# Optimization experiments

Measured on AMD Instinct MI355X. Metric: run time of the kernel, lower is better.

The kernel has to match this reference:

```python
import jax, jax.numpy as jnp
import numpy as np
from jax import lax

D_MODEL = 1024
D_STATE = 16
BATCH = 4
SEQ = 2048
EPS = 1e-5


def setup_inputs() -> dict:
    key = jax.random.key(0)
    ks = jax.random.split(key, 5)
    x = jax.random.normal(ks[0], (BATCH, SEQ, D_MODEL), dtype=jnp.float32)
    A_log = jax.random.normal(ks[1], (D_MODEL, D_STATE), dtype=jnp.float32) * 0.1
    # nn.Linear default init ~ U(-1/sqrt(fan_in), 1/sqrt(fan_in))
    B_w = jax.random.uniform(ks[2], (D_STATE, D_MODEL), minval=-1.0, maxval=1.0) / np.sqrt(D_MODEL)
    C_w = jax.random.uniform(ks[3], (D_MODEL, D_STATE), minval=-1.0, maxval=1.0) / np.sqrt(D_STATE)
    D = jnp.ones((D_MODEL,), dtype=jnp.float32)
    gamma = jnp.ones((D_MODEL,), dtype=jnp.float32)
    beta = jnp.zeros((D_MODEL,), dtype=jnp.float32)
    return {"x": x, "A_log": A_log, "B_w": B_w, "C_w": C_w, "D": D, "gamma": gamma, "beta": beta}


def _layernorm(y, gamma, beta):
    mu = jnp.mean(y, axis=-1, keepdims=True)
    var = jnp.mean((y - mu) ** 2, axis=-1, keepdims=True)
    return (y - mu) * lax.rsqrt(var + EPS) * gamma + beta


def reference(x, A_log, B_w, C_w, D, gamma, beta):
    batch, seq_len, d = x.shape
    decay = jnp.exp(-jnp.exp(A_log))  # (d_model, d_state), exp(A) with A = -exp(A_log)
    # Precompute all B projections: (batch, seq, d_state)
    bx = jnp.einsum('bsd,nd->bsn', x, B_w)
    bx_t = jnp.swapaxes(bx, 0, 1)  # (seq, batch, d_state)

    def step(h, b_t):
        # h: (batch, d_model, d_state); b_t broadcast over d_model dim
        h = h * decay + b_t[:, None, :]
        return h, h.mean(axis=1)  # carry, per-step mean (batch, d_state)

    h0 = jnp.zeros((batch, d, A_log.shape[1]), dtype=x.dtype)
    _, hmeans = lax.scan(step, h0, bx_t)  # hmeans: (seq, batch, d_state)

    y = jnp.einsum('sbn,dn->bsd', hmeans, C_w) + D * x  # (batch, seq, d_model)
    return _layernorm(y, gamma, beta)
```

## Files before the change

kernel.cpp:

```cpp
#include <hip/hip_runtime.h>
#include <hip/hip_bf16.h>

#define D_MODEL 1024
#define D_STATE 16
#define BATCH   4
#define SEQ     2048
#define ROWS    (BATCH*SEQ)
#define WIN     64

#define K1_ROWS 8
__global__ __launch_bounds__(256, 4) void k_bx(const float* __restrict__ x,
                                               const float* __restrict__ Bw,
                                               float* __restrict__ bx) {
    __shared__ float xs[K1_ROWS][1024];
    __shared__ float red[4][8][K1_ROWS][2];
    const int tid  = threadIdx.x;
    const int np   = tid & 7;
    const int dblk = tid >> 3;
    const int row0 = blockIdx.x * K1_ROWS;
    const int lane = tid & 63, wid = tid >> 6;

    float4 bw0[8], bw1[8];
    {
        const float4* p0 = reinterpret_cast<const float4*>(Bw + (size_t)(2 * np    ) * 1024 + dblk * 32);
        const float4* p1 = reinterpret_cast<const float4*>(Bw + (size_t)(2 * np + 1) * 1024 + dblk * 32);
#pragma unroll
        for (int j = 0; j < 8; ++j) { bw0[j] = p0[j]; bw1[j] = p1[j]; }
    }

    const int chunk = tid >> 3;
    const int slotw = ((tid & 7) + chunk) & 7;
#pragma unroll
    for (int r = 0; r < K1_ROWS; ++r) {
        float4 v = reinterpret_cast<const float4*>(x + (size_t)(row0 + r) * 1024)[tid];
        *reinterpret_cast<float4*>(&xs[r][chunk * 32 + slotw * 4]) = v;
    }
    __syncthreads();

    float a0[K1_ROWS], a1[K1_ROWS];
#pragma unroll
    for (int r = 0; r < K1_ROWS; ++r) { a0[r] = 0.f; a1[r] = 0.f; }

#pragma unroll
    for (int r = 0; r < K1_ROWS; ++r) {
#pragma unroll
        for (int j = 0; j < 8; ++j) {
            const int slot = (j + dblk) & 7;
            float4 xv = *reinterpret_cast<const float4*>(&xs[r][dblk * 32 + slot * 4]);
            a0[r] = fmaf(xv.x, bw0[j].x, a0[r]); a0[r] = fmaf(xv.y, bw0[j].y, a0[r]);
            a0[r] = fmaf(xv.z, bw0[j].z, a0[r]); a0[r] = fmaf(xv.w, bw0[j].w, a0[r]);
            a1[r] = fmaf(xv.x, bw1[j].x, a1[r]); a1[r] = fmaf(xv.y, bw1[j].y, a1[r]);
            a1[r] = fmaf(xv.z, bw1[j].z, a1[r]); a1[r] = fmaf(xv.w, bw1[j].w, a1[r]);
        }
    }

#pragma unroll
    for (int r = 0; r < K1_ROWS; ++r) {
        float v0 = a0[r], v1 = a1[r];
        v0 += __shfl_xor(v0, 8);  v1 += __shfl_xor(v1, 8);
        v0 += __shfl_xor(v0, 16); v1 += __shfl_xor(v1, 16);
        v0 += __shfl_xor(v0, 32); v1 += __shfl_xor(v1, 32);
        a0[r] = v0; a1[r] = v1;
    }
    if (lane < 8) {
#pragma unroll
        for (int r = 0; r < K1_ROWS; ++r) {
            red[wid][lane][r][0] = a0[r];
            red[wid][lane][r][1] = a1[r];
        }
    }
    __syncthreads();
    if (tid < K1_ROWS * 16) {
        const int r = tid >> 4, n = tid & 15;
        float v = red[0][n >> 1][r][n & 1] + red[1][n >> 1][r][n & 1]
                + red[2][n >> 1][r][n & 1] + red[3][n >> 1][r][n & 1];
        bx[(size_t)(row0 + r) * D_STATE + n] = v;
    }
}

__global__ __launch_bounds__(256) void k_kbar(const float* __restrict__ A_log,
                                              float* __restrict__ KbarT) {
    const int n = blockIdx.x;
    const int tid = threadIdx.x;
    const int delta = tid & 63;
    const int c     = tid >> 6;
    __shared__ float l2[D_MODEL];
    __shared__ float red[4][WIN];

    for (int d = tid; d < D_MODEL; d += 256) {
        float a = A_log[d * D_STATE + n];
        l2[d] = -expf(a) * 1.4426950408889634f;
    }
    __syncthreads();

    const float fdelta = (float)delta;
    float acc = 0.f;
    const int d0 = c * 256;
    for (int d = d0; d < d0 + 256; ++d)
        acc += exp2f(fdelta * l2[d]);
    red[c][delta] = acc;
    __syncthreads();
    if (tid < WIN)
        KbarT[tid * D_STATE + n] =
            (red[0][tid] + red[1][tid] + red[2][tid] + red[3][tid]) * (1.0f / 1024.0f);
}

__global__ __launch_bounds__(256) void k_fir(const float* __restrict__ bx,
                                             const float* __restrict__ KbarT,
                                             float* __restrict__ hm) {
    __shared__ float4 kb4[WIN][4];
    const int tid = threadIdx.x;
    kb4[tid >> 2][tid & 3] = reinterpret_cast<const float4*>(KbarT)[tid];
    __syncthreads();

    const int nq  = tid & 3;
    const int row = blockIdx.x * 64 + (tid >> 2);
    const int t   = row & (SEQ - 1);
    const float4* bp = reinterpret_cast<const float4*>(bx + (size_t)row * D_STATE) + nq;
    float4 acc = {0.f, 0.f, 0.f, 0.f};
    if (t >= WIN - 1) {
#pragma unroll
        for (int dl = 0; dl < WIN; ++dl) {
            float4 b = bp[-(ptrdiff_t)dl * 4];
            float4 k = kb4[dl][nq];
            acc.x = fmaf(k.x, b.x, acc.x); acc.y = fmaf(k.y, b.y, acc.y);
            acc.z = fmaf(k.z, b.z, acc.z); acc.w = fmaf(k.w, b.w, acc.w);
        }
    } else {
        for (int dl = 0; dl <= t; ++dl) {
            float4 b = bp[-(ptrdiff_t)dl * 4];
            float4 k = kb4[dl][nq];
            acc.x = fmaf(k.x, b.x, acc.x); acc.y = fmaf(k.y, b.y, acc.y);
            acc.z = fmaf(k.z, b.z, acc.z); acc.w = fmaf(k.w, b.w, acc.w);
        }
    }
    reinterpret_cast<float4*>(hm + (size_t)row * D_STATE)[nq] = acc;
}

#define KO_ROWS 4
__global__ __launch_bounds__(256, 4) void k_out(const float* __restrict__ x,
                                                const float* __restrict__ hm,
                                                const float* __restrict__ Cw,
                                                const float* __restrict__ Dp,
                                                const float* __restrict__ gamma,
                                                const float* __restrict__ beta,
                                                float* __restrict__ out) {
    const int tid = threadIdx.x;
    const int row0 = blockIdx.x * KO_ROWS;
    const int lane = tid & 63, wid = tid >> 6;
    __shared__ float red_s[KO_ROWS][4], red_q[KO_ROWS][4];

    float4 cw[4][4];
#pragma unroll
    for (int j = 0; j < 4; ++j) {
        const float4* p = reinterpret_cast<const float4*>(Cw + (size_t)(tid * 4 + j) * D_STATE);
#pragma unroll
        for (int q = 0; q < 4; ++q) cw[j][q] = p[q];
    }
    const float4 Dq = reinterpret_cast<const float4*>(Dp)[tid];
    const float4 gq = reinterpret_cast<const float4*>(gamma)[tid];
    const float4 bq = reinterpret_cast<const float4*>(beta)[tid];

    float4 y[KO_ROWS];
#pragma unroll
    for (int r = 0; r < KO_ROWS; ++r) {
        const size_t row = row0 + r;
        const float4* hp = reinterpret_cast<const float4*>(hm + row * D_STATE);
        const float4 h0 = hp[0], h1 = hp[1], h2 = hp[2], h3 = hp[3];
        const float4 xq = reinterpret_cast<const float4*>(x + row * D_MODEL)[tid];

        float4 v;
#pragma unroll
        for (int j = 0; j < 4; ++j) {
            float a = 0.f;
            a = fmaf(h0.x, cw[j][0].x, a); a = fmaf(h0.y, cw[j][0].y, a);
            a = fmaf(h0.z, cw[j][0].z, a); a = fmaf(h0.w, cw[j][0].w, a);
            a = fmaf(h1.x, cw[j][1].x, a); a = fmaf(h1.y, cw[j][1].y, a);
            a = fmaf(h1.z, cw[j][1].z, a); a = fmaf(h1.w, cw[j][1].w, a);
            a = fmaf(h2.x, cw[j][2].x, a); a = fmaf(h2.y, cw[j][2].y, a);
            a = fmaf(h2.z, cw[j][2].z, a); a = fmaf(h2.w, cw[j][2].w, a);
            a = fmaf(h3.x, cw[j][3].x, a); a = fmaf(h3.y, cw[j][3].y, a);
            a = fmaf(h3.z, cw[j][3].z, a); a = fmaf(h3.w, cw[j][3].w, a);
            ((float*)&v)[j] = a;
        }
        v.x = fmaf(Dq.x, xq.x, v.x);
        v.y = fmaf(Dq.y, xq.y, v.y);
        v.z = fmaf(Dq.z, xq.z, v.z);
        v.w = fmaf(Dq.w, xq.w, v.w);
        y[r] = v;

        float s  = v.x + v.y + v.z + v.w;
        float sq = v.x*v.x + v.y*v.y + v.z*v.z + v.w*v.w;
        s += __shfl_xor(s, 1);  sq += __shfl_xor(sq, 1);
        s += __shfl_xor(s, 2);  sq += __shfl_xor(sq, 2);
        s += __shfl_xor(s, 4);  sq += __shfl_xor(sq, 4);
        s += __shfl_xor(s, 8);  sq += __shfl_xor(sq, 8);
        s += __shfl_xor(s, 16); sq += __shfl_xor(sq, 16);
        s += __shfl_xor(s, 32); sq += __shfl_xor(sq, 32);
        if (lane == 0) { red_s[r][wid] = s; red_q[r][wid] = sq; }
    }
    __syncthreads();

#pragma unroll
    for (int r = 0; r < KO_ROWS; ++r) {
        const size_t row = row0 + r;
        const float ssum = red_s[r][0] + red_s[r][1] + red_s[r][2] + red_s[r][3];
        const float ssq  = red_q[r][0] + red_q[r][1] + red_q[r][2] + red_q[r][3];
        const float mu   = ssum * (1.0f / 1024.0f);
        const float var  = ssq * (1.0f / 1024.0f) - mu * mu;
        const float inv  = rsqrtf(var + 1e-5f);
        const float4 v = y[r];
        float4 o;
        o.x = fmaf((v.x - mu) * inv, gq.x, bq.x);
        o.y = fmaf((v.y - mu) * inv, gq.y, bq.y);
        o.z = fmaf((v.z - mu) * inv, gq.z, bq.z);
        o.w = fmaf((v.w - mu) * inv, gq.w, bq.w);
        reinterpret_cast<float4*>(out + row * D_MODEL)[tid] = o;
    }
}

extern "C" void kernel_launch(void* const* d_in, const int* in_sizes, int n_in,
                              void* d_out, int out_size, void* d_ws, size_t ws_size,
                              hipStream_t stream) {
    (void)in_sizes; (void)n_in; (void)out_size; (void)ws_size;
    const float* x     = (const float*)d_in[0];
    const float* A_log = (const float*)d_in[1];
    const float* B_w   = (const float*)d_in[2];
    const float* C_w   = (const float*)d_in[3];
    const float* Dp    = (const float*)d_in[4];
    const float* gamma = (const float*)d_in[5];
    const float* beta  = (const float*)d_in[6];
    float* out = (float*)d_out;

    float* bx = (float*)d_ws;
    float* kb = bx + (size_t)ROWS * D_STATE;
    float* hm = kb + WIN * D_STATE;

    k_bx  <<<ROWS / K1_ROWS, 256, 0, stream>>>(x, B_w, bx);
    k_kbar<<<D_STATE,        256, 0, stream>>>(A_log, kb);
    k_fir <<<ROWS / 64,      256, 0, stream>>>(bx, kb, hm);
    k_out <<<ROWS / KO_ROWS, 256, 0, stream>>>(x, hm, C_w, Dp, gamma, beta, out);
}
```

Before: 57.76 us.

## Fuse kernel-bar into projection kernel and FIR into output layernorm kernel

Merges the four-kernel pipeline into two launches. The decay-kernel computation now runs as extra blocks of the projection kernel, reusing its shared memory. The FIR convolution over the 64-step window is folded into the output/layernorm kernel, with each block computing its rows' state means into shared memory. This removes two launches and the hm round-trip through global memory, at the cost of redundant kbar loads per block. It also drops the occupancy hint on the projection kernel.

```diff
diff --git a/kernel.cpp b/kernel.cpp
--- a/kernel.cpp
+++ b/kernel.cpp
@@ -9,12 +9,40 @@
 #define WIN     64
 
 #define K1_ROWS 8
-__global__ __launch_bounds__(256, 4) void k_bx(const float* __restrict__ x,
-                                               const float* __restrict__ Bw,
-                                               float* __restrict__ bx) {
+__global__ __launch_bounds__(256) void k_proj(const float* __restrict__ x,
+                                              const float* __restrict__ Bw,
+                                              const float* __restrict__ A_log,
+                                              float* __restrict__ bx,
+                                              float* __restrict__ KbarT) {
     __shared__ float xs[K1_ROWS][1024];
     __shared__ float red[4][8][K1_ROWS][2];
-    const int tid  = threadIdx.x;
+    const int tid = threadIdx.x;
+
+    if (blockIdx.x >= ROWS / K1_ROWS) {
+        const int n = blockIdx.x - ROWS / K1_ROWS;
+        float* l2   = &xs[0][0];
+        float* kred = &xs[1][0];
+        const int delta = tid & 63;
+        const int c     = tid >> 6;
+        for (int d = tid; d < D_MODEL; d += 256) {
+            float a = A_log[d * D_STATE + n];
+            l2[d] = -expf(a) * 1.4426950408889634f;
+        }
+        __syncthreads();
+        const float fdelta = (float)delta;
+        float acc = 0.f;
+        const int d0 = c * 256;
+        for (int d = d0; d < d0 + 256; ++d)
+            acc += exp2f(fdelta * l2[d]);
+        kred[c * WIN + delta] = acc;
+        __syncthreads();
+        if (tid < WIN)
+            KbarT[tid * D_STATE + n] =
+                (kred[tid] + kred[WIN + tid] + kred[2 * WIN + tid] + kred[3 * WIN + tid])
+                * (1.0f / 1024.0f);
+        return;
+    }
+
     const int np   = tid & 7;
     const int dblk = tid >> 3;
     const int row0 = blockIdx.x * K1_ROWS;
@@ -78,77 +106,23 @@
     }
 }
 
-__global__ __launch_bounds__(256) void k_kbar(const float* __restrict__ A_log,
-                                              float* __restrict__ KbarT) {
-    const int n = blockIdx.x;
+#define KB_ROWS 4
+__global__ __launch_bounds__(256, 4) void k_fused(const float* __restrict__ x,
+                                                  const float* __restrict__ bxg,
+                                                  const float* __restrict__ KbarT,
+                                                  const float* __restrict__ Cw,
+                                                  const float* __restrict__ Dp,
+                                                  const float* __restrict__ gamma,
+                                                  const float* __restrict__ beta,
+                                                  float* __restrict__ out) {
     const int tid = threadIdx.x;
-    const int delta = tid & 63;
-    const int c     = tid >> 6;
-    __shared__ float l2[D_MODEL];
-    __shared__ float red[4][WIN];
-
-    for (int d = tid; d < D_MODEL; d += 256) {
-        float a = A_log[d * D_STATE + n];
-        l2[d] = -expf(a) * 1.4426950408889634f;
-    }
-    __syncthreads();
-
-    const float fdelta = (float)delta;
-    float acc = 0.f;
-    const int d0 = c * 256;
-    for (int d = d0; d < d0 + 256; ++d)
-        acc += exp2f(fdelta * l2[d]);
-    red[c][delta] = acc;
-    __syncthreads();
-    if (tid < WIN)
-        KbarT[tid * D_STATE + n] =
-            (red[0][tid] + red[1][tid] + red[2][tid] + red[3][tid]) * (1.0f / 1024.0f);
-}
-
-__global__ __launch_bounds__(256) void k_fir(const float* __restrict__ bx,
-                                             const float* __restrict__ KbarT,
-                                             float* __restrict__ hm) {
-    __shared__ float4 kb4[WIN][4];
-    const int tid = threadIdx.x;
-    kb4[tid >> 2][tid & 3] = reinterpret_cast<const float4*>(KbarT)[tid];
-    __syncthreads();
-
-    const int nq  = tid & 3;
-    const int row = blockIdx.x * 64 + (tid >> 2);
-    const int t   = row & (SEQ - 1);
-    const float4* bp = reinterpret_cast<const float4*>(bx + (size_t)row * D_STATE) + nq;
-    float4 acc = {0.f, 0.f, 0.f, 0.f};
-    if (t >= WIN - 1) {
-#pragma unroll
-        for (int dl = 0; dl < WIN; ++dl) {
-            float4 b = bp[-(ptrdiff_t)dl * 4];
-            float4 k = kb4[dl][nq];
-            acc.x = fmaf(k.x, b.x, acc.x); acc.y = fmaf(k.y, b.y, acc.y);
-            acc.z = fmaf(k.z, b.z, acc.z); acc.w = fmaf(k.w, b.w, acc.w);
-        }
-    } else {
-        for (int dl = 0; dl <= t; ++dl) {
-            float4 b = bp[-(ptrdiff_t)dl * 4];
-            float4 k = kb4[dl][nq];
-            acc.x = fmaf(k.x, b.x, acc.x); acc.y = fmaf(k.y, b.y, acc.y);
-            acc.z = fmaf(k.z, b.z, acc.z); acc.w = fmaf(k.w, b.w, acc.w);
-        }
-    }
-    reinterpret_cast<float4*>(hm + (size_t)row * D_STATE)[nq] = acc;
-}
-
-#define KO_ROWS 4
-__global__ __launch_bounds__(256, 4) void k_out(const float* __restrict__ x,
-                                                const float* __restrict__ hm,
-                                                const float* __restrict__ Cw,
-                                                const float* __restrict__ Dp,
-                                                const float* __restrict__ gamma,
-                                                const float* __restrict__ beta,
-                                                float* __restrict__ out) {
-    const int tid = threadIdx.x;
-    const int row0 = blockIdx.x * KO_ROWS;
+    const int row0 = blockIdx.x * KB_ROWS;
     const int lane = tid & 63, wid = tid >> 6;
-    __shared__ float red_s[KO_ROWS][4], red_q[KO_ROWS][4];
+    __shared__ float kb[WIN * D_STATE];
+    __shared__ float hm_s[KB_ROWS][D_STATE];
+    __shared__ float red_s[KB_ROWS][4], red_q[KB_ROWS][4];
+
+    reinterpret_cast<float4*>(kb)[tid] = reinterpret_cast<const float4*>(KbarT)[tid];
 
     float4 cw[4][4];
 #pragma unroll
@@ -160,12 +134,40 @@
     const float4 Dq = reinterpret_cast<const float4*>(Dp)[tid];
     const float4 gq = reinterpret_cast<const float4*>(gamma)[tid];
     const float4 bq = reinterpret_cast<const float4*>(beta)[tid];
-
-    float4 y[KO_ROWS];
-#pragma unroll
-    for (int r = 0; r < KO_ROWS; ++r) {
+    __syncthreads();
+
+    {
+        const int p = tid >> 2, dc = tid & 3;
+        const int r = p >> 4, n = p & 15;
+        const int row = row0 + r;
+        const int t = row & (SEQ - 1);
+        const float* bp = bxg + (size_t)row * D_STATE + n;
+        float acc = 0.f;
+        if ((row0 & (SEQ - 1)) >= WIN) {
+#pragma unroll
+            for (int j = 0; j < 16; ++j) {
+                const int delta = dc * 16 + j;
+                acc = fmaf(kb[delta * D_STATE + n], bp[-(ptrdiff_t)delta * D_STATE], acc);
+            }
+        } else {
+#pragma unroll
+            for (int j = 0; j < 16; ++j) {
+                const int delta = dc * 16 + j;
+                if (delta <= t)
+                    acc = fmaf(kb[delta * D_STATE + n], bp[-(ptrdiff_t)delta * D_STATE], acc);
+            }
+        }
+        acc += __shfl_xor(acc, 1);
+        acc += __shfl_xor(acc, 2);
+        if (dc == 0) hm_s[r][n] = acc;
+    }
+    __syncthreads();
+
+    float4 y[KB_ROWS];
+#pragma unroll
+    for (int r = 0; r < KB_ROWS; ++r) {
         const size_t row = row0 + r;
-        const float4* hp = reinterpret_cast<const float4*>(hm + row * D_STATE);
+        const float4* hp = reinterpret_cast<const float4*>(&hm_s[r][0]);
         const float4 h0 = hp[0], h1 = hp[1], h2 = hp[2], h3 = hp[3];
         const float4 xq = reinterpret_cast<const float4*>(x + row * D_MODEL)[tid];
 
@@ -202,7 +204,7 @@
     __syncthreads();
 
 #pragma unroll
-    for (int r = 0; r < KO_ROWS; ++r) {
+    for (int r = 0; r < KB_ROWS; ++r) {
         const size_t row = row0 + r;
         const float ssum = red_s[r][0] + red_s[r][1] + red_s[r][2] + red_s[r][3];
         const float ssq  = red_q[r][0] + red_q[r][1] + red_q[r][2] + red_q[r][3];
@@ -234,10 +236,7 @@
 
     float* bx = (float*)d_ws;
     float* kb = bx + (size_t)ROWS * D_STATE;
-    float* hm = kb + WIN * D_STATE;
-
-    k_bx  <<<ROWS / K1_ROWS, 256, 0, stream>>>(x, B_w, bx);
-    k_kbar<<<D_STATE,        256, 0, stream>>>(A_log, kb);
-    k_fir <<<ROWS / 64,      256, 0, stream>>>(bx, kb, hm);
-    k_out <<<ROWS / KO_ROWS, 256, 0, stream>>>(x, hm, C_w, Dp, gamma, beta, out);
+
+    k_proj <<<ROWS / K1_ROWS + D_STATE, 256, 0, stream>>>(x, B_w, A_log, bx, kb);
+    k_fused<<<ROWS / KB_ROWS,           256, 0, stream>>>(x, bx, kb, C_w, Dp, gamma, beta, out);
 }
```

Result: slower. 66.91 us (+15.8%).

## Merge kbar into projection kernel, stage hm in LDS, nontemporal output stores

Applied to the files above, without the earlier changes.

Folds the decay-kernel computation into the B-projection launch as 16 extra blocks, which removes one kernel launch and lets the two run concurrently. In the output kernel, the per-row hm vectors are loaded once into shared memory instead of by every thread. All x loads are issued up front to overlap their latency, and the output is written with nontemporal stores to avoid polluting the cache. The extra blocks reuse the xs shared buffer, and a barrier is added in the output kernel.

```diff
diff --git a/kernel.cpp b/kernel.cpp
--- a/kernel.cpp
+++ b/kernel.cpp
@@ -8,13 +8,43 @@
 #define ROWS    (BATCH*SEQ)
 #define WIN     64
 
+typedef float f32x4 __attribute__((ext_vector_type(4)));
+
 #define K1_ROWS 8
-__global__ __launch_bounds__(256, 4) void k_bx(const float* __restrict__ x,
-                                               const float* __restrict__ Bw,
-                                               float* __restrict__ bx) {
+__global__ __launch_bounds__(256, 4) void k_proj(const float* __restrict__ x,
+                                                 const float* __restrict__ Bw,
+                                                 const float* __restrict__ A_log,
+                                                 float* __restrict__ bx,
+                                                 float* __restrict__ KbarT) {
     __shared__ float xs[K1_ROWS][1024];
     __shared__ float red[4][8][K1_ROWS][2];
-    const int tid  = threadIdx.x;
+    const int tid = threadIdx.x;
+
+    if (blockIdx.x >= ROWS / K1_ROWS) {
+        const int n = blockIdx.x - ROWS / K1_ROWS;
+        float* l2   = &xs[0][0];
+        float* kred = &xs[1][0];
+        const int delta = tid & 63;
+        const int c     = tid >> 6;
+        for (int d = tid; d < D_MODEL; d += 256) {
+            float a = A_log[d * D_STATE + n];
+            l2[d] = -expf(a) * 1.4426950408889634f;
+        }
+        __syncthreads();
+        const float fdelta = (float)delta;
+        float acc = 0.f;
+        const int d0 = c * 256;
+        for (int d = d0; d < d0 + 256; ++d)
+            acc += exp2f(fdelta * l2[d]);
+        kred[c * WIN + delta] = acc;
+        __syncthreads();
+        if (tid < WIN)
+            KbarT[tid * D_STATE + n] =
+                (kred[tid] + kred[WIN + tid] + kred[2 * WIN + tid] + kred[3 * WIN + tid])
+                * (1.0f / 1024.0f);
+        return;
+    }
+
     const int np   = tid & 7;
     const int dblk = tid >> 3;
     const int row0 = blockIdx.x * K1_ROWS;
@@ -76,33 +106,6 @@
                 + red[2][n >> 1][r][n & 1] + red[3][n >> 1][r][n & 1];
         bx[(size_t)(row0 + r) * D_STATE + n] = v;
     }
-}
-
-__global__ __launch_bounds__(256) void k_kbar(const float* __restrict__ A_log,
-                                              float* __restrict__ KbarT) {
-    const int n = blockIdx.x;
-    const int tid = threadIdx.x;
-    const int delta = tid & 63;
-    const int c     = tid >> 6;
-    __shared__ float l2[D_MODEL];
-    __shared__ float red[4][WIN];
-
-    for (int d = tid; d < D_MODEL; d += 256) {
-        float a = A_log[d * D_STATE + n];
-        l2[d] = -expf(a) * 1.4426950408889634f;
-    }
-    __syncthreads();
-
-    const float fdelta = (float)delta;
-    float acc = 0.f;
-    const int d0 = c * 256;
-    for (int d = d0; d < d0 + 256; ++d)
-        acc += exp2f(fdelta * l2[d]);
-    red[c][delta] = acc;
-    __syncthreads();
-    if (tid < WIN)
-        KbarT[tid * D_STATE + n] =
-            (red[0][tid] + red[1][tid] + red[2][tid] + red[3][tid]) * (1.0f / 1024.0f);
 }
 
 __global__ __launch_bounds__(256) void k_fir(const float* __restrict__ bx,
@@ -148,7 +151,17 @@
     const int tid = threadIdx.x;
     const int row0 = blockIdx.x * KO_ROWS;
     const int lane = tid & 63, wid = tid >> 6;
+    __shared__ float4 hm4[KO_ROWS][4];
     __shared__ float red_s[KO_ROWS][4], red_q[KO_ROWS][4];
+
+    if (tid < KO_ROWS * 4)
+        hm4[tid >> 2][tid & 3] =
+            reinterpret_cast<const float4*>(hm + (size_t)(row0 + (tid >> 2)) * D_STATE)[tid & 3];
+
+    float4 xq[KO_ROWS];
+#pragma unroll
+    for (int r = 0; r < KO_ROWS; ++r)
+        xq[r] = reinterpret_cast<const float4*>(x + (size_t)(row0 + r) * D_MODEL)[tid];
 
     float4 cw[4][4];
 #pragma unroll
@@ -160,15 +173,12 @@
     const float4 Dq = reinterpret_cast<const float4*>(Dp)[tid];
     const float4 gq = reinterpret_cast<const float4*>(gamma)[tid];
     const float4 bq = reinterpret_cast<const float4*>(beta)[tid];
+    __syncthreads();
 
     float4 y[KO_ROWS];
 #pragma unroll
     for (int r = 0; r < KO_ROWS; ++r) {
-        const size_t row = row0 + r;
-        const float4* hp = reinterpret_cast<const float4*>(hm + row * D_STATE);
-        const float4 h0 = hp[0], h1 = hp[1], h2 = hp[2], h3 = hp[3];
-        const float4 xq = reinterpret_cast<const float4*>(x + row * D_MODEL)[tid];
-
+        const float4 h0 = hm4[r][0], h1 = hm4[r][1], h2 = hm4[r][2], h3 = hm4[r][3];
         float4 v;
 #pragma unroll
         for (int j = 0; j < 4; ++j) {
@@ -183,10 +193,10 @@
             a = fmaf(h3.z, cw[j][3].z, a); a = fmaf(h3.w, cw[j][3].w, a);
             ((float*)&v)[j] = a;
         }
-        v.x = fmaf(Dq.x, xq.x, v.x);
-        v.y = fmaf(Dq.y, xq.y, v.y);
-        v.z = fmaf(Dq.z, xq.z, v.z);
-        v.w = fmaf(Dq.w, xq.w, v.w);
+        v.x = fmaf(Dq.x, xq[r].x, v.x);
+        v.y = fmaf(Dq.y, xq[r].y, v.y);
+        v.z = fmaf(Dq.z, xq[r].z, v.z);
+        v.w = fmaf(Dq.w, xq[r].w, v.w);
         y[r] = v;
 
         float s  = v.x + v.y + v.z + v.w;
@@ -210,12 +220,12 @@
         const float var  = ssq * (1.0f / 1024.0f) - mu * mu;
         const float inv  = rsqrtf(var + 1e-5f);
         const float4 v = y[r];
-        float4 o;
+        f32x4 o;
         o.x = fmaf((v.x - mu) * inv, gq.x, bq.x);
         o.y = fmaf((v.y - mu) * inv, gq.y, bq.y);
         o.z = fmaf((v.z - mu) * inv, gq.z, bq.z);
         o.w = fmaf((v.w - mu) * inv, gq.w, bq.w);
-        reinterpret_cast<float4*>(out + row * D_MODEL)[tid] = o;
+        __builtin_nontemporal_store(o, reinterpret_cast<f32x4*>(out + row * D_MODEL) + tid);
     }
 }
 
@@ -236,8 +246,7 @@
     float* kb = bx + (size_t)ROWS * D_STATE;
     float* hm = kb + WIN * D_STATE;
 
-    k_bx  <<<ROWS / K1_ROWS, 256, 0, stream>>>(x, B_w, bx);
-    k_kbar<<<D_STATE,        256, 0, stream>>>(A_log, kb);
-    k_fir <<<ROWS / 64,      256, 0, stream>>>(bx, kb, hm);
-    k_out <<<ROWS / KO_ROWS, 256, 0, stream>>>(x, hm, C_w, Dp, gamma, beta, out);
-}
+    k_proj<<<ROWS / K1_ROWS + D_STATE, 256, 0, stream>>>(x, B_w, A_log, bx, kb);
+    k_fir <<<ROWS / 64,                256, 0, stream>>>(bx, kb, hm);
+    k_out <<<ROWS / KO_ROWS,           256, 0, stream>>>(x, hm, C_w, Dp, gamma, beta, out);
+}
```

Measured after the change: 63.97 us. 10.7% more time.
